# Kernel optimization log

Measured on AMD Instinct MI355X. Metric: run time of the kernel, lower is better.

## Reference

```python
import jax, jax.numpy as jnp
import numpy as np

EPS = 1e-5  # torch LayerNorm default


def setup_inputs() -> dict:
    key = jax.random.key(0)
    ks = jax.random.split(key, 12)
    N, D, F = 4096, 1024, 4096
    s = 1.0 / np.sqrt(D)
    sf = 1.0 / np.sqrt(F)
    return {
        "embeddings": jax.random.normal(ks[0], (N, D), dtype=jnp.float32),
        "Wq": jax.random.normal(ks[1], (D, D), dtype=jnp.float32) * s,
        "bq": jnp.zeros((D,), jnp.float32),
        "Wk": jax.random.normal(ks[2], (D, D), dtype=jnp.float32) * s,
        "bk": jnp.zeros((D,), jnp.float32),
        "Wv": jax.random.normal(ks[3], (D, D), dtype=jnp.float32) * s,
        "bv": jnp.zeros((D,), jnp.float32),
        "gamma": jnp.ones((D,), jnp.float32),
        "beta": jnp.zeros((D,), jnp.float32),
        "W1": jax.random.normal(ks[4], (D, F), dtype=jnp.float32) * s,
        "b1": jnp.zeros((F,), jnp.float32),
        "W2": jax.random.normal(ks[5], (F, D), dtype=jnp.float32) * sf,
        "b2": jnp.zeros((D,), jnp.float32),
    }


def reference(embeddings, Wq, bq, Wk, bk, Wv, bv, gamma, beta, W1, b1, W2, b2):
    N, D = embeddings.shape
    scale = jnp.sqrt(jnp.float32(D))  # embed_dim ** 0.5
    Q = embeddings @ Wq + bq          # [N, D]
    K = embeddings @ Wk + bk
    V = embeddings @ Wv + bv
    attn = (Q @ K.T) / scale          # [N, N]
    # causal mask: strictly upper triangle -> -inf
    causal = jnp.tril(jnp.ones((N, N), dtype=bool))
    attn = jnp.where(causal, attn, -jnp.inf)
    A = jax.nn.softmax(attn, axis=-1)
    attn_emb = A @ V                  # [N, D]  (dropout = identity at eval)
    # add & norm (LayerNorm over last dim)
    x = attn_emb + embeddings
    mu = jnp.mean(x, axis=-1, keepdims=True)
    var = jnp.mean((x - mu) ** 2, axis=-1, keepdims=True)
    x = (x - mu) / jnp.sqrt(var + EPS) * gamma + beta
    # FFN (no residual after ff in the original module)
    h = jax.nn.relu(x @ W1 + b1)
    return h @ W2 + b2
```

## Files before the change

### kernel.cpp

```cpp
#include <hip/hip_runtime.h>
#include <stdint.h>


using short8 = __attribute__((ext_vector_type(8))) short;
using f32x4  = __attribute__((ext_vector_type(4))) float;

__device__ __forceinline__ uint16_t f2bf(float f) {
  uint32_t u = __builtin_bit_cast(uint32_t, f);
  u += 0x7FFFu + ((u >> 16) & 1u);
  return (uint16_t)(u >> 16);
}

__device__ __forceinline__ void gload_lds16(const uint16_t* g, uint16_t* l) {
  __builtin_amdgcn_global_load_lds(
      (__attribute__((address_space(1))) void*)(void*)g,
      (__attribute__((address_space(3))) void*)l, 16, 0, 0);
}


__global__ __launch_bounds__(256) void gemm_bt(
    const uint16_t* __restrict__ A, const uint16_t* __restrict__ Bt,
    const float* __restrict__ bias, void* __restrict__ Cout,
    int K, int lda, int ldb, int ldc,
    float scale, int out_bf16, int relu, int mode)
{
  constexpr int BK = 64;
  __shared__ uint16_t As[128 * BK];
  __shared__ uint16_t Bs[128 * BK];
  int bm, bn, half = 0, klo = 0, khi = K;
  if (mode == 3) {
    bn = blockIdx.x; bm = blockIdx.y >> 1; half = blockIdx.y & 1;
    int mid = K >> 1; klo = half ? mid : 0; khi = half ? K : mid;
  } else {
    bm = blockIdx.y; bn = blockIdx.x;
  }

  int tid  = threadIdx.x;
  int lane = tid & 63;
  int wave = tid >> 6;
  int wm = (wave >> 1) * 64, wn = (wave & 1) * 64;
  int lr = lane & 15, quad = lane >> 4;

  const uint16_t *Ag[4], *Bg[4];
  uint16_t *Al[4], *Bl[4];
#pragma unroll
  for (int s = 0; s < 4; ++s) {
    int c = tid + 256 * s;
    int r = c >> 3, q = (c & 7) ^ (r & 7);
    Ag[s] = A  + (size_t)(bm * 128 + r) * lda + q * 8;
    Bg[s] = Bt + (size_t)(bn * 128 + r) * ldb + q * 8;
    Al[s] = As + c * 8;
    Bl[s] = Bs + c * 8;
  }

  f32x4 acc[4][4] = {};

  for (int k0 = klo; k0 < khi; k0 += BK) {
    __syncthreads();
#pragma unroll
    for (int s = 0; s < 4; ++s) gload_lds16(Ag[s] + k0, Al[s]);
#pragma unroll
    for (int s = 0; s < 4; ++s) gload_lds16(Bg[s] + k0, Bl[s]);
    __syncthreads();
#pragma unroll
    for (int h = 0; h < 2; ++h) {
      short8 af[4], bfr[4];
      int cc = quad + 4 * h;
#pragma unroll
      for (int i = 0; i < 4; ++i) {
        int r = wm + i * 16 + lr;
        af[i] = *(const short8*)(&As[(r * 8 + (cc ^ (r & 7))) * 8]);
      }
#pragma unroll
      for (int j = 0; j < 4; ++j) {
        int r = wn + j * 16 + lr;
        bfr[j] = *(const short8*)(&Bs[(r * 8 + (cc ^ (r & 7))) * 8]);
      }
#pragma unroll
      for (int i = 0; i < 4; ++i)
#pragma unroll
        for (int j = 0; j < 4; ++j)
          acc[i][j] = __builtin_amdgcn_mfma_f32_16x16x32_bf16(af[i], bfr[j], acc[i][j], 0, 0, 0);
    }
  }

  void* Cw = (mode == 3) ? (void*)((float*)Cout + (size_t)half * 4096 * ldc) : Cout;
  int row0 = bm * 128 + wm + quad * 4;
  int col0 = bn * 128 + wn + lr;
#pragma unroll
  for (int j = 0; j < 4; ++j) {
    int col = col0 + j * 16;
    float bv = bias ? bias[col] : 0.0f;
#pragma unroll
    for (int i = 0; i < 4; ++i) {
#pragma unroll
      for (int r = 0; r < 4; ++r) {
        int row = row0 + i * 16 + r;
        float v = acc[i][j][r] * scale + bv;
        if (relu) v = fmaxf(v, 0.0f);
        size_t idx = (size_t)row * ldc + col;
        if (out_bf16) ((uint16_t*)Cw)[idx] = f2bf(v);
        else          ((float*)Cw)[idx]    = v;
      }
    }
  }
}

__global__ __launch_bounds__(256) void gemm_s(
    const uint16_t* __restrict__ Qm, const uint16_t* __restrict__ Km,
    uint16_t* __restrict__ Sb, int lda, int ldb, int ldc, float scale)
{
  constexpr int BK = 64;
  __shared__ uint16_t As[64 * BK];
  __shared__ uint16_t Bs[128 * BK];
  int t = blockIdx.x;
  int u = (int)sqrtf((float)t);
  while ((u + 1) * (u + 1) <= t) ++u;
  while (u * u > t) --u;
  int i64, bn;
  if (t < u * (u + 1)) { i64 = 2 * u - 1; bn = t - u * u; }
  else                 { i64 = 2 * u;     bn = t - u * (u + 1); }

  int tid  = threadIdx.x;
  int lane = tid & 63;
  int wave = tid >> 6;
  int wm = (wave >> 1) * 32, wn = (wave & 1) * 64;
  int lr = lane & 15, quad = lane >> 4;

  const uint16_t *Ag[2], *Bg[4];
  uint16_t *Al[2], *Bl[4];
#pragma unroll
  for (int s = 0; s < 2; ++s) {
    int c = tid + 256 * s;
    int r = c >> 3, q = (c & 7) ^ (r & 7);
    Ag[s] = Qm + (size_t)(i64 * 64 + r) * lda + q * 8;
    Al[s] = As + c * 8;
  }
#pragma unroll
  for (int s = 0; s < 4; ++s) {
    int c = tid + 256 * s;
    int r = c >> 3, q = (c & 7) ^ (r & 7);
    Bg[s] = Km + (size_t)(bn * 128 + r) * ldb + q * 8;
    Bl[s] = Bs + c * 8;
  }

  f32x4 acc[2][4] = {};

  for (int k0 = 0; k0 < 1024; k0 += BK) {
    __syncthreads();
#pragma unroll
    for (int s = 0; s < 2; ++s) gload_lds16(Ag[s] + k0, Al[s]);
#pragma unroll
    for (int s = 0; s < 4; ++s) gload_lds16(Bg[s] + k0, Bl[s]);
    __syncthreads();
#pragma unroll
    for (int h = 0; h < 2; ++h) {
      short8 af[2], bfr[4];
      int cc = quad + 4 * h;
#pragma unroll
      for (int i = 0; i < 2; ++i) {
        int r = wm + i * 16 + lr;
        af[i] = *(const short8*)(&As[(r * 8 + (cc ^ (r & 7))) * 8]);
      }
#pragma unroll
      for (int j = 0; j < 4; ++j) {
        int r = wn + j * 16 + lr;
        bfr[j] = *(const short8*)(&Bs[(r * 8 + (cc ^ (r & 7))) * 8]);
      }
#pragma unroll
      for (int i = 0; i < 2; ++i)
#pragma unroll
        for (int j = 0; j < 4; ++j)
          acc[i][j] = __builtin_amdgcn_mfma_f32_16x16x32_bf16(af[i], bfr[j], acc[i][j], 0, 0, 0);
    }
  }

  int row0 = i64 * 64 + wm + quad * 4;
  int col0 = bn * 128 + wn + lr;
#pragma unroll
  for (int j = 0; j < 4; ++j) {
    int col = col0 + j * 16;
#pragma unroll
    for (int i = 0; i < 2; ++i) {
#pragma unroll
      for (int r = 0; r < 4; ++r) {
        int row = row0 + i * 16 + r;
        float v = (col <= row) ? __expf(acc[i][j][r] * scale) : 0.0f;
        Sb[(size_t)row * ldc + col] = f2bf(v);
      }
    }
  }
}

__global__ __launch_bounds__(256) void gemm_bt_n64(
    const uint16_t* __restrict__ A, const uint16_t* __restrict__ Bt,
    const float* __restrict__ bias, void* __restrict__ Cout,
    int K, int lda, int ldb, int ldc,
    float scale, int out_bf16, int relu, int mode)
{
  constexpr int BK = 64;
  __shared__ uint16_t As[128 * BK];
  __shared__ uint16_t Bs[64 * BK];
  int bn = blockIdx.x, b = blockIdx.y;
  int bm, half = 0, klo = 0, khi = K;
  if (mode == 2) {
    int t = b >> 1; half = b & 1;
    bm = (t & 1) ? (t >> 1) : (31 - (t >> 1));
    int kmax = (bm + 1) << 7, mid = kmax >> 1;
    klo = half ? mid : 0; khi = half ? kmax : mid;
  } else if (mode == 3) {
    bm = b >> 1; half = b & 1;
    int mid = K >> 1; klo = half ? mid : 0; khi = half ? K : mid;
  } else {
    bm = b;
  }

  int tid  = threadIdx.x;
  int lane = tid & 63;
  int wave = tid >> 6;
  int wm = (wave & 1) * 64, wn = (wave >> 1) * 32;
  int lr = lane & 15, quad = lane >> 4;

  const uint16_t *Ag[4], *Bg[2];
  uint16_t *Al[4], *Bl[2];
#pragma unroll
  for (int s = 0; s < 4; ++s) {
    int c = tid + 256 * s;
    int r = c >> 3, q = (c & 7) ^ (r & 7);
    Ag[s] = A + (size_t)(bm * 128 + r) * lda + q * 8;
    Al[s] = As + c * 8;
  }
#pragma unroll
  for (int s = 0; s < 2; ++s) {
    int c = tid + 256 * s;
    int r = c >> 3, q = (c & 7) ^ (r & 7);
    Bg[s] = Bt + (size_t)(bn * 64 + r) * ldb + q * 8;
    Bl[s] = Bs + c * 8;
  }

  f32x4 acc[4][2] = {};

  for (int k0 = klo; k0 < khi; k0 += BK) {
    __syncthreads();
#pragma unroll
    for (int s = 0; s < 4; ++s) gload_lds16(Ag[s] + k0, Al[s]);
#pragma unroll
    for (int s = 0; s < 2; ++s) gload_lds16(Bg[s] + k0, Bl[s]);
    __syncthreads();
#pragma unroll
    for (int h = 0; h < 2; ++h) {
      short8 af[4], bfr[2];
      int cc = quad + 4 * h;
#pragma unroll
      for (int i = 0; i < 4; ++i) {
        int r = wm + i * 16 + lr;
        af[i] = *(const short8*)(&As[(r * 8 + (cc ^ (r & 7))) * 8]);
      }
#pragma unroll
      for (int j = 0; j < 2; ++j) {
        int r = wn + j * 16 + lr;
        bfr[j] = *(const short8*)(&Bs[(r * 8 + (cc ^ (r & 7))) * 8]);
      }
#pragma unroll
      for (int i = 0; i < 4; ++i)
#pragma unroll
        for (int j = 0; j < 2; ++j)
          acc[i][j] = __builtin_amdgcn_mfma_f32_16x16x32_bf16(af[i], bfr[j], acc[i][j], 0, 0, 0);
    }
  }

  void* Cw = (mode >= 2) ? (void*)((float*)Cout + (size_t)half * 4096 * ldc) : Cout;
  int row0 = bm * 128 + wm + quad * 4;
  int col0 = bn * 64 + wn + lr;
#pragma unroll
  for (int j = 0; j < 2; ++j) {
    int col = col0 + j * 16;
    float bv = bias ? bias[col] : 0.0f;
#pragma unroll
    for (int i = 0; i < 4; ++i) {
#pragma unroll
      for (int r = 0; r < 4; ++r) {
        int row = row0 + i * 16 + r;
        float v = acc[i][j][r] * scale + bv;
        if (relu) v = fmaxf(v, 0.0f);
        size_t idx = (size_t)row * ldc + col;
        if (out_bf16) ((uint16_t*)Cw)[idx] = f2bf(v);
        else          ((float*)Cw)[idx]    = v;
      }
    }
  }
}

__device__ __forceinline__ float block_sum(float v, float* red) {
#pragma unroll
  for (int o = 32; o > 0; o >>= 1) v += __shfl_xor(v, o, 64);
  if ((threadIdx.x & 63) == 0) red[threadIdx.x >> 6] = v;
  __syncthreads();
  v = red[0] + red[1] + red[2] + red[3];
  __syncthreads();
  return v;
}

__global__ __launch_bounds__(256) void rowsum_exp(
    const uint16_t* __restrict__ Sb, float* __restrict__ l)
{
  __shared__ float red[4];
  int i = blockIdx.x, tid = threadIdx.x;
  const ushort4* row = (const ushort4*)(Sb + (size_t)i * 4096);
  int lim4 = (((i >> 7) + 1) << 7) >> 2;
  float s = 0.0f;
  for (int c = tid; c < lim4; c += 256) {
    ushort4 u = row[c];
    s += __builtin_bit_cast(float, (uint32_t)u.x << 16)
       + __builtin_bit_cast(float, (uint32_t)u.y << 16)
       + __builtin_bit_cast(float, (uint32_t)u.z << 16)
       + __builtin_bit_cast(float, (uint32_t)u.w << 16);
  }
  s = block_sum(s, red);
  if (tid == 0) l[i] = s;
}

__global__ __launch_bounds__(256) void add_layernorm(
    const float* __restrict__ P, const float* __restrict__ l,
    const float* __restrict__ emb, const float* __restrict__ gamma,
    const float* __restrict__ beta, uint16_t* __restrict__ xB)
{
  __shared__ float red[4];
  int i = blockIdx.x, tid = threadIdx.x;
  float inv_l = 1.0f / l[i];
  float4 a0 = ((const float4*)(P + (size_t)i * 1024))[tid];
  float4 a1 = ((const float4*)(P + 4194304 + (size_t)i * 1024))[tid];
  float4 b  = ((const float4*)(emb + (size_t)i * 1024))[tid];
  float x0 = (a0.x + a1.x) * inv_l + b.x, x1 = (a0.y + a1.y) * inv_l + b.y;
  float x2 = (a0.z + a1.z) * inv_l + b.z, x3 = (a0.w + a1.w) * inv_l + b.w;
  float mu = block_sum(x0 + x1 + x2 + x3, red) * (1.0f / 1024.0f);
  float d0 = x0 - mu, d1 = x1 - mu, d2 = x2 - mu, d3 = x3 - mu;
  float var = block_sum(d0 * d0 + d1 * d1 + d2 * d2 + d3 * d3, red) * (1.0f / 1024.0f);
  float rs = rsqrtf(var + 1e-5f);
  float4 g  = ((const float4*)gamma)[tid];
  float4 be = ((const float4*)beta)[tid];
  ushort4 o;
  o.x = f2bf(d0 * rs * g.x + be.x);
  o.y = f2bf(d1 * rs * g.y + be.y);
  o.z = f2bf(d2 * rs * g.z + be.z);
  o.w = f2bf(d3 * rs * g.w + be.w);
  ((ushort4*)(xB + (size_t)i * 1024))[tid] = o;
}

__global__ __launch_bounds__(256) void reduce2_bias(
    const float* __restrict__ P, const float* __restrict__ bias,
    float* __restrict__ out)
{
  int i = blockIdx.x, tid = threadIdx.x;
  float4 a = ((const float4*)(P + (size_t)i * 1024))[tid];
  float4 c = ((const float4*)(P + 4194304 + (size_t)i * 1024))[tid];
  float4 bv = ((const float4*)bias)[tid];
  float4 o;
  o.x = a.x + c.x + bv.x; o.y = a.y + c.y + bv.y;
  o.z = a.z + c.z + bv.z; o.w = a.w + c.w + bv.w;
  ((float4*)(out + (size_t)i * 1024))[tid] = o;
}

__global__ __launch_bounds__(256) void cast_f32_bf16(
    const float* __restrict__ in, uint16_t* __restrict__ out, int n4)
{
  int idx = blockIdx.x * 256 + threadIdx.x;
  if (idx >= n4) return;
  float4 v = ((const float4*)in)[idx];
  ushort4 o; o.x = f2bf(v.x); o.y = f2bf(v.y); o.z = f2bf(v.z); o.w = f2bf(v.w);
  ((ushort4*)out)[idx] = o;
}

__global__ __launch_bounds__(256) void cast_transpose(
    const float* __restrict__ in, uint16_t* __restrict__ out, int R, int C)
{
  __shared__ float tile[32][33];
  int tx = threadIdx.x & 31, ty = threadIdx.x >> 5;
  int r0 = blockIdx.y * 32, c0 = blockIdx.x * 32;
#pragma unroll
  for (int r = 0; r < 32; r += 8)
    tile[ty + r][tx] = in[(size_t)(r0 + ty + r) * C + c0 + tx];
  __syncthreads();
#pragma unroll
  for (int r = 0; r < 32; r += 8)
    out[(size_t)(c0 + ty + r) * R + r0 + tx] = f2bf(tile[tx][ty + r]);
}

__global__ __launch_bounds__(256) void cast_transpose_qkv(
    const float* __restrict__ Wq, const float* __restrict__ Wk,
    const float* __restrict__ Wv, uint16_t* __restrict__ out)
{
  __shared__ float tile[32][33];
  const float* in = (blockIdx.z == 0) ? Wq : (blockIdx.z == 1) ? Wk : Wv;
  uint16_t* o = out + (size_t)blockIdx.z * 1048576;
  int tx = threadIdx.x & 31, ty = threadIdx.x >> 5;
  int r0 = blockIdx.y * 32, c0 = blockIdx.x * 32;
#pragma unroll
  for (int r = 0; r < 32; r += 8)
    tile[ty + r][tx] = in[(size_t)(r0 + ty + r) * 1024 + c0 + tx];
  __syncthreads();
#pragma unroll
  for (int r = 0; r < 32; r += 8)
    o[(size_t)(c0 + ty + r) * 1024 + r0 + tx] = f2bf(tile[tx][ty + r]);
}

__global__ __launch_bounds__(256) void transpose_u16(
    const uint16_t* __restrict__ in, uint16_t* __restrict__ out, int R, int C, int ldin)
{
  __shared__ uint16_t tile[32][33];
  int tx = threadIdx.x & 31, ty = threadIdx.x >> 5;
  int r0 = blockIdx.y * 32, c0 = blockIdx.x * 32;
#pragma unroll
  for (int r = 0; r < 32; r += 8)
    tile[ty + r][tx] = in[(size_t)(r0 + ty + r) * ldin + c0 + tx];
  __syncthreads();
#pragma unroll
  for (int r = 0; r < 32; r += 8)
    out[(size_t)(c0 + ty + r) * R + r0 + tx] = tile[tx][ty + r];
}

__global__ __launch_bounds__(256) void pack_bias3(
    const float* __restrict__ b0, const float* __restrict__ b1,
    const float* __restrict__ b2, float* __restrict__ out)
{
  int i = blockIdx.x * 256 + threadIdx.x;
  float v = (i < 1024) ? b0[i] : (i < 2048) ? b1[i - 1024] : b2[i - 2048];
  out[i] = v;
}

extern "C" void kernel_launch(void* const* d_in, const int* in_sizes, int n_in,
                              void* d_out, int out_size, void* d_ws, size_t ws_size,
                              hipStream_t stream) {
  const float* emb   = (const float*)d_in[0];
  const float* Wq    = (const float*)d_in[1];
  const float* bq    = (const float*)d_in[2];
  const float* Wk    = (const float*)d_in[3];
  const float* bk    = (const float*)d_in[4];
  const float* Wv    = (const float*)d_in[5];
  const float* bv    = (const float*)d_in[6];
  const float* gamma = (const float*)d_in[7];
  const float* beta  = (const float*)d_in[8];
  const float* W1    = (const float*)d_in[9];
  const float* b1    = (const float*)d_in[10];
  const float* W2    = (const float*)d_in[11];
  const float* b2    = (const float*)d_in[12];

  char* w = (char*)d_ws;
  const size_t MB = 1ull << 20;
  uint16_t* embB  = (uint16_t*)(w + 0 * MB);
  uint16_t* WqkvT = (uint16_t*)(w + 8 * MB);
  uint16_t* W1T   = (uint16_t*)(w + 14 * MB);
  uint16_t* W2T   = (uint16_t*)(w + 22 * MB);
  float*    bqkv  = (float*)(w + 30 * MB);
  float*    lvec  = (float*)(w + 30 * MB + 65536);
  uint16_t* QKVb  = (uint16_t*)(w + 31 * MB);
  uint16_t* Vt    = (uint16_t*)(w + 55 * MB);
  uint16_t* xB    = (uint16_t*)(w + 0 * MB);
  uint16_t* hB    = (uint16_t*)(w + 63 * MB);
  uint16_t* Sb    = (uint16_t*)(w + 95 * MB);
  float*    Opart = (float*)(w + 63 * MB);
  float*    Fpart = (float*)(w + 127 * MB);

  cast_f32_bf16     <<<4096, 256, 0, stream>>>(emb, embB, 1024 * 1024);
  cast_transpose_qkv<<<dim3(32, 32, 3), 256, 0, stream>>>(Wq, Wk, Wv, WqkvT);
  cast_transpose    <<<dim3(128, 32), 256, 0, stream>>>(W1, W1T, 1024, 4096);
  cast_transpose    <<<dim3(32, 128), 256, 0, stream>>>(W2, W2T, 4096, 1024);
  pack_bias3        <<<12, 256, 0, stream>>>(bq, bk, bv, bqkv);

  gemm_bt<<<dim3(24, 32), 256, 0, stream>>>(embB, WqkvT, bqkv, QKVb,
      1024, 1024, 1024, 3072, 1.0f, 1, 0, 0);
  const uint16_t* Qb = QKVb;
  const uint16_t* Kb = QKVb + 1024;
  const uint16_t* Vb = QKVb + 2048;
  transpose_u16<<<dim3(32, 128), 256, 0, stream>>>(Vb, Vt, 4096, 1024, 3072);

  gemm_s<<<1056, 256, 0, stream>>>(Qb, Kb, Sb, 3072, 3072, 4096, 0.03125f);
  rowsum_exp<<<4096, 256, 0, stream>>>(Sb, lvec);
  gemm_bt_n64<<<dim3(16, 64), 256, 0, stream>>>(Sb, Vt, nullptr, Opart,
      4096, 4096, 4096, 1024, 1.0f, 0, 0, 2);

  add_layernorm<<<4096, 256, 0, stream>>>(Opart, lvec, emb, gamma, beta, xB);
  gemm_bt<<<dim3(32, 32), 256, 0, stream>>>(xB, W1T, b1, hB,
      1024, 1024, 1024, 4096, 1.0f, 1, 1, 0);
  gemm_bt_n64<<<dim3(16, 64), 256, 0, stream>>>(hB, W2T, nullptr, Fpart,
      4096, 4096, 4096, 1024, 1.0f, 0, 0, 3);
  reduce2_bias<<<4096, 256, 0, stream>>>(Fpart, b2, (float*)d_out);
}
```

Measured before the change: 366.3 us.

## Fuse prep kernels, V transpose, rowsum and split-K reduction into neighbouring kernels

Merges the five weight/input cast and transpose launches into one prep kernel, which also zeroes the row-sum vector and initialises the output with b2. The QKV GEMM epilogue now writes V directly in transposed layout, removing the separate transpose kernel. The softmax row sums are accumulated in the score GEMM epilogue with wave shuffles and atomics, replacing the rowsum kernel. The FFN2 split-K halves atomically add into the bias-initialised output, replacing the partial buffer and reduce kernel. This cuts launches and memory round trips but adds strided transposed stores and float atomics that make accumulation order non-deterministic.

```diff
diff --git a/kernel.cpp b/kernel.cpp
--- a/kernel.cpp
+++ b/kernel.cpp
@@ -21,19 +21,14 @@
 __global__ __launch_bounds__(256) void gemm_bt(
     const uint16_t* __restrict__ A, const uint16_t* __restrict__ Bt,
     const float* __restrict__ bias, void* __restrict__ Cout,
+    uint16_t* __restrict__ VtOut,
     int K, int lda, int ldb, int ldc,
-    float scale, int out_bf16, int relu, int mode)
+    float scale, int out_bf16, int relu)
 {
   constexpr int BK = 64;
   __shared__ uint16_t As[128 * BK];
   __shared__ uint16_t Bs[128 * BK];
-  int bm, bn, half = 0, klo = 0, khi = K;
-  if (mode == 3) {
-    bn = blockIdx.x; bm = blockIdx.y >> 1; half = blockIdx.y & 1;
-    int mid = K >> 1; klo = half ? mid : 0; khi = half ? K : mid;
-  } else {
-    bm = blockIdx.y; bn = blockIdx.x;
-  }
+  int bm = blockIdx.y, bn = blockIdx.x;
 
   int tid  = threadIdx.x;
   int lane = tid & 63;
@@ -55,7 +50,7 @@
 
   f32x4 acc[4][4] = {};
 
-  for (int k0 = klo; k0 < khi; k0 += BK) {
+  for (int k0 = 0; k0 < K; k0 += BK) {
     __syncthreads();
 #pragma unroll
     for (int s = 0; s < 4; ++s) gload_lds16(Ag[s] + k0, Al[s]);
@@ -84,7 +79,6 @@
     }
   }
 
-  void* Cw = (mode == 3) ? (void*)((float*)Cout + (size_t)half * 4096 * ldc) : Cout;
   int row0 = bm * 128 + wm + quad * 4;
   int col0 = bn * 128 + wn + lr;
 #pragma unroll
@@ -98,9 +92,13 @@
         int row = row0 + i * 16 + r;
         float v = acc[i][j][r] * scale + bv;
         if (relu) v = fmaxf(v, 0.0f);
-        size_t idx = (size_t)row * ldc + col;
-        if (out_bf16) ((uint16_t*)Cw)[idx] = f2bf(v);
-        else          ((float*)Cw)[idx]    = v;
+        if (VtOut && col >= 2048) {
+          VtOut[(size_t)(col - 2048) * 4096 + row] = f2bf(v);
+        } else {
+          size_t idx = (size_t)row * ldc + col;
+          if (out_bf16) ((uint16_t*)Cout)[idx] = f2bf(v);
+          else          ((float*)Cout)[idx]    = v;
+        }
       }
     }
   }
@@ -108,7 +106,8 @@
 
 __global__ __launch_bounds__(256) void gemm_s(
     const uint16_t* __restrict__ Qm, const uint16_t* __restrict__ Km,
-    uint16_t* __restrict__ Sb, int lda, int ldb, int ldc, float scale)
+    uint16_t* __restrict__ Sb, float* __restrict__ lvec,
+    int lda, int ldb, int ldc, float scale)
 {
   constexpr int BK = 64;
   __shared__ uint16_t As[64 * BK];
@@ -178,25 +177,29 @@
   int row0 = i64 * 64 + wm + quad * 4;
   int col0 = bn * 128 + wn + lr;
 #pragma unroll
-  for (int j = 0; j < 4; ++j) {
-    int col = col0 + j * 16;
-#pragma unroll
-    for (int i = 0; i < 2; ++i) {
-#pragma unroll
-      for (int r = 0; r < 4; ++r) {
-        int row = row0 + i * 16 + r;
+  for (int i = 0; i < 2; ++i) {
+#pragma unroll
+    for (int r = 0; r < 4; ++r) {
+      int row = row0 + i * 16 + r;
+      float s = 0.0f;
+#pragma unroll
+      for (int j = 0; j < 4; ++j) {
+        int col = col0 + j * 16;
         float v = (col <= row) ? __expf(acc[i][j][r] * scale) : 0.0f;
         Sb[(size_t)row * ldc + col] = f2bf(v);
-      }
+        s += v;
+      }
+#pragma unroll
+      for (int o = 8; o > 0; o >>= 1) s += __shfl_xor(s, o, 64);
+      if (lr == 0) unsafeAtomicAdd(&lvec[row], s);
     }
   }
 }
 
 __global__ __launch_bounds__(256) void gemm_bt_n64(
     const uint16_t* __restrict__ A, const uint16_t* __restrict__ Bt,
-    const float* __restrict__ bias, void* __restrict__ Cout,
-    int K, int lda, int ldb, int ldc,
-    float scale, int out_bf16, int relu, int mode)
+    void* __restrict__ Cout,
+    int K, int lda, int ldb, int ldc, int mode)
 {
   constexpr int BK = 64;
   __shared__ uint16_t As[128 * BK];
@@ -208,11 +211,9 @@
     bm = (t & 1) ? (t >> 1) : (31 - (t >> 1));
     int kmax = (bm + 1) << 7, mid = kmax >> 1;
     klo = half ? mid : 0; khi = half ? kmax : mid;
-  } else if (mode == 3) {
+  } else {
     bm = b >> 1; half = b & 1;
     int mid = K >> 1; klo = half ? mid : 0; khi = half ? K : mid;
-  } else {
-    bm = b;
   }
 
   int tid  = threadIdx.x;
@@ -269,25 +270,30 @@
     }
   }
 
-  void* Cw = (mode >= 2) ? (void*)((float*)Cout + (size_t)half * 4096 * ldc) : Cout;
   int row0 = bm * 128 + wm + quad * 4;
   int col0 = bn * 64 + wn + lr;
-#pragma unroll
-  for (int j = 0; j < 2; ++j) {
-    int col = col0 + j * 16;
-    float bv = bias ? bias[col] : 0.0f;
-#pragma unroll
-    for (int i = 0; i < 4; ++i) {
-#pragma unroll
-      for (int r = 0; r < 4; ++r) {
-        int row = row0 + i * 16 + r;
-        float v = acc[i][j][r] * scale + bv;
-        if (relu) v = fmaxf(v, 0.0f);
-        size_t idx = (size_t)row * ldc + col;
-        if (out_bf16) ((uint16_t*)Cw)[idx] = f2bf(v);
-        else          ((float*)Cw)[idx]    = v;
-      }
-    }
+  if (mode == 4) {
+    float* Cw = (float*)Cout;
+#pragma unroll
+    for (int j = 0; j < 2; ++j)
+#pragma unroll
+      for (int i = 0; i < 4; ++i)
+#pragma unroll
+        for (int r = 0; r < 4; ++r) {
+          size_t idx = (size_t)(row0 + i * 16 + r) * ldc + col0 + j * 16;
+          unsafeAtomicAdd(&Cw[idx], acc[i][j][r]);
+        }
+  } else {
+    float* Cw = (float*)Cout + (size_t)half * 4096 * ldc;
+#pragma unroll
+    for (int j = 0; j < 2; ++j)
+#pragma unroll
+      for (int i = 0; i < 4; ++i)
+#pragma unroll
+        for (int r = 0; r < 4; ++r) {
+          size_t idx = (size_t)(row0 + i * 16 + r) * ldc + col0 + j * 16;
+          Cw[idx] = acc[i][j][r];
+        }
   }
 }
 
@@ -299,25 +305,6 @@
   v = red[0] + red[1] + red[2] + red[3];
   __syncthreads();
   return v;
-}
-
-__global__ __launch_bounds__(256) void rowsum_exp(
-    const uint16_t* __restrict__ Sb, float* __restrict__ l)
-{
-  __shared__ float red[4];
-  int i = blockIdx.x, tid = threadIdx.x;
-  const ushort4* row = (const ushort4*)(Sb + (size_t)i * 4096);
-  int lim4 = (((i >> 7) + 1) << 7) >> 2;
-  float s = 0.0f;
-  for (int c = tid; c < lim4; c += 256) {
-    ushort4 u = row[c];
-    s += __builtin_bit_cast(float, (uint32_t)u.x << 16)
-       + __builtin_bit_cast(float, (uint32_t)u.y << 16)
-       + __builtin_bit_cast(float, (uint32_t)u.z << 16)
-       + __builtin_bit_cast(float, (uint32_t)u.w << 16);
-  }
-  s = block_sum(s, red);
-  if (tid == 0) l[i] = s;
 }
 
 __global__ __launch_bounds__(256) void add_layernorm(
@@ -347,85 +334,81 @@
   ((ushort4*)(xB + (size_t)i * 1024))[tid] = o;
 }
 
-__global__ __launch_bounds__(256) void reduce2_bias(
-    const float* __restrict__ P, const float* __restrict__ bias,
-    float* __restrict__ out)
-{
-  int i = blockIdx.x, tid = threadIdx.x;
-  float4 a = ((const float4*)(P + (size_t)i * 1024))[tid];
-  float4 c = ((const float4*)(P + 4194304 + (size_t)i * 1024))[tid];
-  float4 bv = ((const float4*)bias)[tid];
-  float4 o;
-  o.x = a.x + c.x + bv.x; o.y = a.y + c.y + bv.y;
-  o.z = a.z + c.z + bv.z; o.w = a.w + c.w + bv.w;
-  ((float4*)(out + (size_t)i * 1024))[tid] = o;
-}
-
-__global__ __launch_bounds__(256) void cast_f32_bf16(
-    const float* __restrict__ in, uint16_t* __restrict__ out, int n4)
-{
-  int idx = blockIdx.x * 256 + threadIdx.x;
-  if (idx >= n4) return;
-  float4 v = ((const float4*)in)[idx];
-  ushort4 o; o.x = f2bf(v.x); o.y = f2bf(v.y); o.z = f2bf(v.z); o.w = f2bf(v.w);
-  ((ushort4*)out)[idx] = o;
-}
-
-__global__ __launch_bounds__(256) void cast_transpose(
-    const float* __restrict__ in, uint16_t* __restrict__ out, int R, int C)
+__global__ __launch_bounds__(256) void prep(
+    const float* __restrict__ emb, const float* __restrict__ Wq,
+    const float* __restrict__ Wk, const float* __restrict__ Wv,
+    const float* __restrict__ W1, const float* __restrict__ W2,
+    const float* __restrict__ bq, const float* __restrict__ bk,
+    const float* __restrict__ bv, const float* __restrict__ b2,
+    uint16_t* __restrict__ embB, uint16_t* __restrict__ WqkvT,
+    uint16_t* __restrict__ W1T, uint16_t* __restrict__ W2T,
+    float* __restrict__ bqkv, float* __restrict__ lvec,
+    float* __restrict__ outInit)
 {
   __shared__ float tile[32][33];
-  int tx = threadIdx.x & 31, ty = threadIdx.x >> 5;
-  int r0 = blockIdx.y * 32, c0 = blockIdx.x * 32;
-#pragma unroll
-  for (int r = 0; r < 32; r += 8)
-    tile[ty + r][tx] = in[(size_t)(r0 + ty + r) * C + c0 + tx];
-  __syncthreads();
-#pragma unroll
-  for (int r = 0; r < 32; r += 8)
-    out[(size_t)(c0 + ty + r) * R + r0 + tx] = f2bf(tile[tx][ty + r]);
-}
-
-__global__ __launch_bounds__(256) void cast_transpose_qkv(
-    const float* __restrict__ Wq, const float* __restrict__ Wk,
-    const float* __restrict__ Wv, uint16_t* __restrict__ out)
-{
-  __shared__ float tile[32][33];
-  const float* in = (blockIdx.z == 0) ? Wq : (blockIdx.z == 1) ? Wk : Wv;
-  uint16_t* o = out + (size_t)blockIdx.z * 1048576;
-  int tx = threadIdx.x & 31, ty = threadIdx.x >> 5;
-  int r0 = blockIdx.y * 32, c0 = blockIdx.x * 32;
-#pragma unroll
-  for (int r = 0; r < 32; r += 8)
-    tile[ty + r][tx] = in[(size_t)(r0 + ty + r) * 1024 + c0 + tx];
-  __syncthreads();
-#pragma unroll
-  for (int r = 0; r < 32; r += 8)
-    o[(size_t)(c0 + ty + r) * 1024 + r0 + tx] = f2bf(tile[tx][ty + r]);
-}
-
-__global__ __launch_bounds__(256) void transpose_u16(
-    const uint16_t* __restrict__ in, uint16_t* __restrict__ out, int R, int C, int ldin)
-{
-  __shared__ uint16_t tile[32][33];
-  int tx = threadIdx.x & 31, ty = threadIdx.x >> 5;
-  int r0 = blockIdx.y * 32, c0 = blockIdx.x * 32;
-#pragma unroll
-  for (int r = 0; r < 32; r += 8)
-    tile[ty + r][tx] = in[(size_t)(r0 + ty + r) * ldin + c0 + tx];
-  __syncthreads();
-#pragma unroll
-  for (int r = 0; r < 32; r += 8)
-    out[(size_t)(c0 + ty + r) * R + r0 + tx] = tile[tx][ty + r];
-}
-
-__global__ __launch_bounds__(256) void pack_bias3(
-    const float* __restrict__ b0, const float* __restrict__ b1,
-    const float* __restrict__ b2, float* __restrict__ out)
-{
-  int i = blockIdx.x * 256 + threadIdx.x;
-  float v = (i < 1024) ? b0[i] : (i < 2048) ? b1[i - 1024] : b2[i - 2048];
-  out[i] = v;
+  int b = blockIdx.x, tid = threadIdx.x;
+  if (b < 4096) {
+    int idx = b * 256 + tid;
+    float4 v = ((const float4*)emb)[idx];
+    ushort4 o; o.x = f2bf(v.x); o.y = f2bf(v.y); o.z = f2bf(v.z); o.w = f2bf(v.w);
+    ((ushort4*)embB)[idx] = o;
+    return;
+  }
+  int tx = tid & 31, ty = tid >> 5;
+  if (b < 7168) {
+    int local = b - 4096;
+    const float* in = (local < 1024) ? Wq : (local < 2048) ? Wk : Wv;
+    uint16_t* o = WqkvT + (size_t)(local >> 10) * 1048576;
+    int rem = local & 1023;
+    int r0 = (rem >> 5) * 32, c0 = (rem & 31) * 32;
+#pragma unroll
+    for (int r = 0; r < 32; r += 8)
+      tile[ty + r][tx] = in[(size_t)(r0 + ty + r) * 1024 + c0 + tx];
+    __syncthreads();
+#pragma unroll
+    for (int r = 0; r < 32; r += 8)
+      o[(size_t)(c0 + ty + r) * 1024 + r0 + tx] = f2bf(tile[tx][ty + r]);
+    return;
+  }
+  if (b < 11264) {
+    int local = b - 7168;
+    int c0 = (local & 127) * 32, r0 = (local >> 7) * 32;
+#pragma unroll
+    for (int r = 0; r < 32; r += 8)
+      tile[ty + r][tx] = W1[(size_t)(r0 + ty + r) * 4096 + c0 + tx];
+    __syncthreads();
+#pragma unroll
+    for (int r = 0; r < 32; r += 8)
+      W1T[(size_t)(c0 + ty + r) * 1024 + r0 + tx] = f2bf(tile[tx][ty + r]);
+    return;
+  }
+  if (b < 15360) {
+    int local = b - 11264;
+    int c0 = (local & 31) * 32, r0 = (local >> 5) * 32;
+#pragma unroll
+    for (int r = 0; r < 32; r += 8)
+      tile[ty + r][tx] = W2[(size_t)(r0 + ty + r) * 1024 + c0 + tx];
+    __syncthreads();
+#pragma unroll
+    for (int r = 0; r < 32; r += 8)
+      W2T[(size_t)(c0 + ty + r) * 4096 + r0 + tx] = f2bf(tile[tx][ty + r]);
+    return;
+  }
+  if (b < 15372) {
+    int i = (b - 15360) * 256 + tid;
+    bqkv[i] = (i < 1024) ? bq[i] : (i < 2048) ? bk[i - 1024] : bv[i - 2048];
+    return;
+  }
+  if (b == 15372) {
+#pragma unroll
+    for (int i = tid; i < 4096; i += 256) lvec[i] = 0.0f;
+    return;
+  }
+  {
+    int row = b - 15373;
+    float4 bv4 = ((const float4*)b2)[tid];
+    ((float4*)(outInit + (size_t)row * 1024))[tid] = bv4;
+  }
 }
 
 extern "C" void kernel_launch(void* const* d_in, const int* in_sizes, int n_in,
@@ -459,30 +442,26 @@
   uint16_t* hB    = (uint16_t*)(w + 63 * MB);
   uint16_t* Sb    = (uint16_t*)(w + 95 * MB);
   float*    Opart = (float*)(w + 63 * MB);
-  float*    Fpart = (float*)(w + 127 * MB);
-
-  cast_f32_bf16     <<<4096, 256, 0, stream>>>(emb, embB, 1024 * 1024);
-  cast_transpose_qkv<<<dim3(32, 32, 3), 256, 0, stream>>>(Wq, Wk, Wv, WqkvT);
-  cast_transpose    <<<dim3(128, 32), 256, 0, stream>>>(W1, W1T, 1024, 4096);
-  cast_transpose    <<<dim3(32, 128), 256, 0, stream>>>(W2, W2T, 4096, 1024);
-  pack_bias3        <<<12, 256, 0, stream>>>(bq, bk, bv, bqkv);
-
-  gemm_bt<<<dim3(24, 32), 256, 0, stream>>>(embB, WqkvT, bqkv, QKVb,
-      1024, 1024, 1024, 3072, 1.0f, 1, 0, 0);
+
+  prep<<<19469, 256, 0, stream>>>(emb, Wq, Wk, Wv, W1, W2, bq, bk, bv, b2,
+                                  embB, WqkvT, W1T, W2T, bqkv, lvec,
+                                  (float*)d_out);
+
+  gemm_bt<<<dim3(24, 32), 256, 0, stream>>>(embB, WqkvT, bqkv, QKVb, Vt,
+      1024, 1024, 1024, 3072, 1.0f, 1, 0);
   const uint16_t* Qb = QKVb;
   const uint16_t* Kb = QKVb + 1024;
-  const uint16_t* Vb = QKVb + 2048;
-  transpose_u16<<<dim3(32, 128), 256, 0, stream>>>(Vb, Vt, 4096, 1024, 3072);
-
-  gemm_s<<<1056, 256, 0, stream>>>(Qb, Kb, Sb, 3072, 3072, 4096, 0.03125f);
-  rowsum_exp<<<4096, 256, 0, stream>>>(Sb, lvec);
-  gemm_bt_n64<<<dim3(16, 64), 256, 0, stream>>>(Sb, Vt, nullptr, Opart,
-      4096, 4096, 4096, 1024, 1.0f, 0, 0, 2);
+
+  gemm_s<<<1056, 256, 0, stream>>>(Qb, Kb, Sb, lvec, 3072, 3072, 4096, 0.03125f);
+
+  gemm_bt_n64<<<dim3(16, 64), 256, 0, stream>>>(Sb, Vt, Opart,
+      4096, 4096, 4096, 1024, 2);
 
   add_layernorm<<<4096, 256, 0, stream>>>(Opart, lvec, emb, gamma, beta, xB);
-  gemm_bt<<<dim3(32, 32), 256, 0, stream>>>(xB, W1T, b1, hB,
-      1024, 1024, 1024, 4096, 1.0f, 1, 1, 0);
-  gemm_bt_n64<<<dim3(16, 64), 256, 0, stream>>>(hB, W2T, nullptr, Fpart,
-      4096, 4096, 4096, 1024, 1.0f, 0, 0, 3);
-  reduce2_bias<<<4096, 256, 0, stream>>>(Fpart, b2, (float*)d_out);
-}
+
+  gemm_bt<<<dim3(32, 32), 256, 0, stream>>>(xB, W1T, b1, hB, nullptr,
+      1024, 1024, 1024, 4096, 1.0f, 1, 1);
+
+  gemm_bt_n64<<<dim3(16, 64), 256, 0, stream>>>(hB, W2T, d_out,
+      4096, 4096, 4096, 1024, 4);
+}
```

Result: no change. 364.0 us (-0.6%).
